# Kernel tuning notes

Measured on AMD Instinct MI355X. Metric: run time of the kernel, lower is better.

The kernel has to match this reference:

```python
import jax, jax.numpy as jnp
import numpy as np

EPS = 1e-6
NUM_HEADS = 12


def ln_cf(x, w, b):
    # channels_first LayerNorm over channel dim (ConvNeXt style)
    u = jnp.mean(x, axis=1, keepdims=True)
    s = jnp.mean((x - u) ** 2, axis=1, keepdims=True)
    xn = (x - u) / jnp.sqrt(s + EPS)
    shp = (1, -1) + (1,) * (x.ndim - 2)
    return xn * w.reshape(shp) + b.reshape(shp)


def conv2s2(x, w):
    # Conv3d kernel=2 stride=2 (no bias): exact non-overlapping patch contraction
    b, c, H, W, D = x.shape
    xp = x.reshape(b, c, H // 2, 2, W // 2, 2, D // 2, 2)
    return jnp.einsum('bchkwpdq,ockpq->bohwd', xp, w)


def convt2s2(x, w):
    # ConvTranspose3d kernel=2 stride=2 (torch weight layout [in, out, 2,2,2])
    b, i, H, W, D = x.shape
    o = w.shape[1]
    y = jnp.einsum('bihwd,iokpq->bohkwpdq', x, w)
    return y.reshape(b, o, 2 * H, 2 * W, 2 * D)


def stem(x, w1, g1, b1, w2, g2, b2):
    h = conv2s2(x, w1)
    h = jax.nn.gelu(ln_cf(h, g1, b1), approximate=False)
    h = conv2s2(h, w2)
    return ln_cf(h, g2, b2)


def debed(x, tw1, g, b, tw2, tb2):
    h = convt2s2(x, tw1)
    h = jax.nn.gelu(ln_cf(h, g, b), approximate=False)
    return convt2s2(h, tw2) + tb2.reshape(1, -1, 1, 1, 1)


def rope(x):
    # rotary embedding over full token dim c (pairs (i, i+c/2)), positions 0..L-1
    b, l, c = x.shape
    inv = 1.0 / (10000.0 ** (jnp.arange(0, c, 2, dtype=jnp.float32) / c))
    t = jnp.arange(l, dtype=jnp.float32)
    f = jnp.outer(t, inv)                      # [l, c/2]
    emb = jnp.concatenate([f, f], axis=-1)     # [l, c]
    cos, sin = jnp.cos(emb)[None], jnp.sin(emb)[None]
    rot = jnp.concatenate([-x[..., c // 2:], x[..., :c // 2]], axis=-1)
    return x * cos + rot * sin


def _forward(x, skip, q_w1, q_g1, q_b1, q_w2, q_g2, q_b2,
             k_w1, k_g1, k_b1, k_w2, k_g2, k_b2,
             v_w1, v_g1, v_b1, v_w2, v_g2, v_b2,
             o_tw1, o_g, o_b, o_tw2, o_tb2,
             ns_w, ns_b, nx_w, nx_b, no_w, no_b):
    res = skip
    skip = ln_cf(skip, ns_w, ns_b)
    x = ln_cf(x, nx_w, nx_b)
    q = stem(skip, q_w1, q_g1, q_b1, q_w2, q_g2, q_b2)
    k = stem(x, k_w1, k_g1, k_b1, k_w2, k_g2, k_b2)
    v = stem(x, v_w1, v_g1, v_b1, v_w2, v_g2, v_b2)
    b, c, Hq, Wq, Dq = q.shape
    _, _, Hk, Wk, Dk = k.shape
    q = q.reshape(b, c, -1).transpose(0, 2, 1)   # [b, Lq, c]
    k = k.reshape(b, c, -1).transpose(0, 2, 1)   # [b, Lk, c]
    v = v.reshape(b, c, -1).transpose(0, 2, 1)
    q = rope(q)
    k = rope(k)
    hd = c // NUM_HEADS
    qh = q.reshape(b, -1, NUM_HEADS, hd).transpose(0, 2, 1, 3)  # [b, nh, Lq, hd]
    kh = k.reshape(b, -1, NUM_HEADS, hd).transpose(0, 2, 1, 3)
    vh = v.reshape(b, -1, NUM_HEADS, hd).transpose(0, 2, 1, 3)
    scale = 1.0 / jnp.sqrt(jnp.float32(hd))
    attn = jax.nn.softmax(jnp.einsum('bhqc,bhkc->bhqk', qh, kh) * scale, axis=-1)
    proj = jnp.einsum('bhqk,bhkc->bhqc', attn, vh)              # [b, nh, Lq, hd]
    # rearrange 'b nh l c -> b (c nh) h w d'
    proj = proj.transpose(0, 3, 1, 2).reshape(b, c, Hq, Wq, Dq)
    proj = ln_cf(proj, no_w, no_b)
    out = debed(proj, o_tw1, o_g, o_b, o_tw2, o_tb2)
    return out + res


def setup_inputs() -> dict:
    key = jax.random.key(0)
    ks = iter(jax.random.split(key, 40))
    def nrm(shape, scale):
        return jax.random.normal(next(ks), shape, jnp.float32) * scale
    E, E4, XF, SF = 768, 192, 6, 6
    inp = {
        'x': nrm((2, XF, 48, 48, 48), 1.0),
        'skip': nrm((2, SF, 48, 48, 48), 1.0),
    }
    for p, ic in [('q', SF), ('k', XF), ('v', XF)]:
        inp[p + '_w1'] = nrm((E4, ic, 2, 2, 2), (ic * 8) ** -0.5)
        inp[p + '_g1'] = jnp.ones(E4, jnp.float32)
        inp[p + '_b1'] = jnp.zeros(E4, jnp.float32)
        inp[p + '_w2'] = nrm((E, E4, 2, 2, 2), (E4 * 8) ** -0.5)
        inp[p + '_g2'] = jnp.ones(E, jnp.float32)
        inp[p + '_b2'] = jnp.zeros(E, jnp.float32)
    inp['o_tw1'] = nrm((E, E4, 2, 2, 2), E ** -0.5)
    inp['o_g'] = jnp.ones(E4, jnp.float32)
    inp['o_b'] = jnp.zeros(E4, jnp.float32)
    inp['o_tw2'] = nrm((E4, SF, 2, 2, 2), E4 ** -0.5)
    inp['o_tb2'] = jnp.zeros(SF, jnp.float32)
    inp['ns_w'] = jnp.ones(SF, jnp.float32)
    inp['ns_b'] = jnp.zeros(SF, jnp.float32)
    inp['nx_w'] = jnp.ones(XF, jnp.float32)
    inp['nx_b'] = jnp.zeros(XF, jnp.float32)
    inp['no_w'] = jnp.ones(E, jnp.float32)
    inp['no_b'] = jnp.zeros(E, jnp.float32)
    return inp


def reference(x, skip, q_w1, q_g1, q_b1, q_w2, q_g2, q_b2,
              k_w1, k_g1, k_b1, k_w2, k_g2, k_b2,
              v_w1, v_g1, v_b1, v_w2, v_g2, v_b2,
              o_tw1, o_g, o_b, o_tw2, o_tb2,
              ns_w, ns_b, nx_w, nx_b, no_w, no_b):
    return _forward(x, skip, q_w1, q_g1, q_b1, q_w2, q_g2, q_b2,
                    k_w1, k_g1, k_b1, k_w2, k_g2, k_b2,
                    v_w1, v_g1, v_b1, v_w2, v_g2, v_b2,
                    o_tw1, o_g, o_b, o_tw2, o_tb2,
                    ns_w, ns_b, nx_w, nx_b, no_w, no_b)
```

## Files before the change

### kernel.cpp

```cpp
#include <hip/hip_runtime.h>
#include <math.h>

#define BB_ 2
#define C0 6
#define S0 48
#define V0 (S0*S0*S0)
#define C1 192
#define S1 24
#define V1 (S1*S1*S1)
#define C2 768
#define S2 12
#define LL (S2*S2*S2)
#define NH 12
#define HD 64
#define KDIM (C1*8)
#define MDIM (BB_*LL)

typedef __attribute__((ext_vector_type(8))) short short8;
typedef __attribute__((ext_vector_type(4))) short short4v;
typedef __attribute__((ext_vector_type(4))) float float4v;

static __device__ __forceinline__ float gelu_exact(float x){
  return 0.5f*x*(1.0f+erff(x*0.70710678118654752440f));
}
static __device__ __forceinline__ unsigned short f2bf(float f){
  unsigned int u = __float_as_uint(f);
  unsigned int r = (u + 0x7fffu + ((u>>16)&1u)) >> 16;
  return (unsigned short)r;
}
static __device__ __forceinline__ unsigned int pk_bf16(float a, float b){
#if __has_builtin(__builtin_amdgcn_cvt_pk_bf16_f32)
  typedef __attribute__((ext_vector_type(2))) __bf16 bf2;
  bf2 r = __builtin_amdgcn_cvt_pk_bf16_f32(a,b);
  union { bf2 v; unsigned int u; } cv; cv.v = r;
  return cv.u;
#else
  return (unsigned int)f2bf(a) | ((unsigned int)f2bf(b)<<16);
#endif
}
static __device__ __forceinline__ float bf2f(unsigned short u){
  return __uint_as_float(((unsigned int)u)<<16);
}
static __device__ __forceinline__ float exp2v(float x){
#if __has_builtin(__builtin_amdgcn_exp2f)
  return __builtin_amdgcn_exp2f(x);
#else
  return exp2f(x);
#endif
}
static __device__ __forceinline__ void load_lds16(const void* g, void* l){
  __builtin_amdgcn_global_load_lds((const __attribute__((address_space(1))) unsigned int*)g,
      (__attribute__((address_space(3))) unsigned int*)l, 16, 0, 0);
}
static __device__ __forceinline__ float4v mfma32(short8 a, short8 b, float4v c){
  return __builtin_amdgcn_mfma_f32_16x16x32_bf16(a,b,c,0,0,0);
}
static __device__ __forceinline__ float4v mfma16(short4v a, short4v b, float4v c){
#if __has_builtin(__builtin_amdgcn_mfma_f32_16x16x16bf16_1k)
  return __builtin_amdgcn_mfma_f32_16x16x16bf16_1k(a,b,c,0,0,0);
#else
  asm volatile("v_mfma_f32_16x16x16_bf16 %0, %1, %2, %0" : "+v"(c) : "v"(a), "v"(b));
  return c;
#endif
}

__global__ __launch_bounds__(256) void prep_kernel(
    const float* __restrict__ skin, const float* __restrict__ xin,
    const float* __restrict__ nsw, const float* __restrict__ nsb,
    const float* __restrict__ nxw, const float* __restrict__ nxb,
    unsigned short* __restrict__ outS, unsigned short* __restrict__ outX,
    const float* __restrict__ qw2, const float* __restrict__ kw2, const float* __restrict__ vw2,
    const float* __restrict__ tw1, const float* __restrict__ tw2,
    const float* __restrict__ qw1, const float* __restrict__ kw1, const float* __restrict__ vw1,
    unsigned short* __restrict__ w2tq, unsigned short* __restrict__ w2tk,
    unsigned short* __restrict__ w2tv, unsigned short* __restrict__ Btd,
    unsigned short* __restrict__ Bt48,
    unsigned short* __restrict__ w1q, unsigned short* __restrict__ w1k,
    unsigned short* __restrict__ w1v){
  int bx = blockIdx.x;
  if (bx < 1728){
    int z = bx >= 864;
    const float* in = z ? xin : skin;
    const float* w  = z ? nxw : nsw;
    const float* bi = z ? nxb : nsb;
    unsigned short* out = z ? outX : outS;
    int idx = (bx - z*864)*256 + threadIdx.x;
    int b = idx / V0, vox = idx - b*V0;
    const float* p = in + (size_t)b*(C0*V0) + vox;
    float v[C0]; float s=0.f;
#pragma unroll
    for (int c=0;c<C0;c++){ v[c]=p[(size_t)c*V0]; s+=v[c]; }
    float u = s*(1.f/C0);
    float ss=0.f;
#pragma unroll
    for (int c=0;c<C0;c++){ float d=v[c]-u; ss+=d*d; }
    float inv = rsqrtf(ss*(1.f/C0)+1e-6f);
    unsigned short* o = out + (size_t)b*(C0*V0) + vox;
#pragma unroll
    for (int c=0;c<C0;c++) o[(size_t)c*V0] = f2bf((v[c]-u)*inv*w[c]+bi[c]);
    return;
  }
  bx -= 1728;
  if (bx < 13824){
    int z = bx/4608;
    int idx = (bx - z*4608)*256 + threadIdx.x;
    const float* w2 = (z==0)?qw2:((z==1)?kw2:vw2);
    unsigned short* o = (z==0)?w2tq:((z==1)?w2tk:w2tv);
    int oc = idx/KDIM; int r = idx-oc*KDIM; int p = r/C1; int ic = r-p*C1;
    o[idx] = f2bf(w2[(size_t)oc*KDIM + ic*8 + p]);
  } else if (bx < 18432){
    int idx = (bx-13824)*256 + threadIdx.x;
    int n = idx/C2; int p = idx-n*C2;
    int i = ((p&63)*NH) + (p>>6);
    int kpq = n/C1, o2 = n-kpq*C1;
    Btd[idx] = f2bf(tw1[(size_t)i*KDIM + o2*8 + kpq]);
  } else if (bx < 18480){
    int idx = (bx-18432)*256 + threadIdx.x;
    int n = idx/C1; int i = idx-n*C1;
    Bt48[idx] = (n<48) ? f2bf(tw2[(size_t)i*48 + n]) : (unsigned short)0;
  } else {
    int idx = (bx-18480)*256 + threadIdx.x;
    int z = idx / 9216; int r = idx - z*9216;
    const float* w1 = (z==0)?qw1:((z==1)?kw1:vw1);
    unsigned short* o = (z==0)?w1q:((z==1)?w1k:w1v);
    o[r] = f2bf(w1[r]);
  }
}

__global__ __launch_bounds__(256) void conv1_kernel(
    const unsigned short* __restrict__ lnSb, const unsigned short* __restrict__ lnXb,
    const unsigned short* __restrict__ w1bq, const unsigned short* __restrict__ w1bk,
    const unsigned short* __restrict__ w1bv,
    const float* __restrict__ qg1, const float* __restrict__ qb1,
    const float* __restrict__ kg1, const float* __restrict__ kb1,
    const float* __restrict__ vg1, const float* __restrict__ vb1,
    unsigned short* __restrict__ h1q, unsigned short* __restrict__ h1k,
    unsigned short* __restrict__ h1v){
  int z = blockIdx.z;
  const unsigned short* in = (z==0)? lnSb : lnXb;
  const unsigned short* Wb = (z==0)?w1bq:((z==1)?w1bk:w1bv);
  const float* g1 = (z==0)?qg1:((z==1)?kg1:vg1);
  const float* b1 = (z==0)?qb1:((z==1)?kb1:vb1);
  unsigned short* h1p = (z==0)?h1q:((z==1)?h1k:h1v);
  int t = threadIdx.x, w = t>>6, lane = t&63;
  int g = lane>>4, l16 = lane&15;
  int j = blockIdx.x*4 + w;
  int bxh = j/18, mt = j - bxh*18;
  int b = bxh/48; int rem = bxh - b*48; int y = rem>>1, xh = rem&1;
  int xo = mt/3, zo = mt - xo*3;
  int xv = xh*12 + xo*2 + (l16>>3);
  int zv = zo*8 + (l16&7);
  int x2 = 2*xv, z2 = 2*zv, y2 = 2*y;
  const unsigned short* base = in + (size_t)b*C0*V0;
  union { short8 v; unsigned int u[4]; } aA;
  {
    size_t rb = (size_t)g*V0;
    aA.u[0] = *(const unsigned int*)&base[rb + (y2+0)*(S0*S0) + (x2+0)*S0 + z2];
    aA.u[1] = *(const unsigned int*)&base[rb + (y2+0)*(S0*S0) + (x2+1)*S0 + z2];
    aA.u[2] = *(const unsigned int*)&base[rb + (y2+1)*(S0*S0) + (x2+0)*S0 + z2];
    aA.u[3] = *(const unsigned int*)&base[rb + (y2+1)*(S0*S0) + (x2+1)*S0 + z2];
  }
  union { short4v v; unsigned int u[2]; } aB;
  {
    size_t rb = (size_t)(4+(g>>1))*V0 + (y2+(g&1))*(S0*S0);
    aB.u[0] = *(const unsigned int*)&base[rb + (x2+0)*S0 + z2];
    aB.u[1] = *(const unsigned int*)&base[rb + (x2+1)*S0 + z2];
  }
  float4v acc[12];
#pragma unroll
  for (int ot=0; ot<12; ot++){
    short8  wA = *(const short8*)&Wb[(ot*16+l16)*48 + g*8];
    short4v wB = *(const short4v*)&Wb[(ot*16+l16)*48 + 32 + g*4];
    float4v a = {};
    a = mfma32(wA, aA.v, a);
    a = mfma16(wB, aB.v, a);
    acc[ot] = a;
  }
  float s1=0.f, s2=0.f;
#pragma unroll
  for (int ot=0;ot<12;ot++)
#pragma unroll
    for (int reg=0;reg<4;reg++){ float v=acc[ot][reg]; s1+=v; s2+=v*v; }
  s1 += __shfl_xor(s1,16); s1 += __shfl_xor(s1,32);
  s2 += __shfl_xor(s2,16); s2 += __shfl_xor(s2,32);
  float u = s1*(1.f/C1);
  float inv = rsqrtf(s2*(1.f/C1)-u*u+1e-6f);
  int tok = (y>>1)*(S2*S2) + (xv>>1)*S2 + (zv>>1);
  int p8 = (y&1)*4 + (xv&1)*2 + (zv&1);
  unsigned short* hb = h1p + (size_t)(b*LL+tok)*KDIM + p8*C1;
#pragma unroll
  for (int ot=0; ot<12; ot++){
    int oc0 = ot*16 + g*4;
    float4 gg = *(const float4*)&g1[oc0];
    float4 bb = *(const float4*)&b1[oc0];
    float x0 = gelu_exact((acc[ot][0]-u)*inv*gg.x+bb.x);
    float x1 = gelu_exact((acc[ot][1]-u)*inv*gg.y+bb.y);
    float x2e= gelu_exact((acc[ot][2]-u)*inv*gg.z+bb.z);
    float x3 = gelu_exact((acc[ot][3]-u)*inv*gg.w+bb.w);
    uint2 pk; pk.x = pk_bf16(x0,x1); pk.y = pk_bf16(x2e,x3);
    *(uint2*)&hb[oc0] = pk;
  }
}

__global__ __launch_bounds__(256) void gemm_stem_kernel(
    const unsigned short* __restrict__ A0, const unsigned short* __restrict__ A1,
    const unsigned short* __restrict__ A2,
    const unsigned short* __restrict__ B0, const unsigned short* __restrict__ B1,
    const unsigned short* __restrict__ B2,
    unsigned short* __restrict__ Cq, unsigned short* __restrict__ Ck,
    unsigned short* __restrict__ Cv){
  int flat = blockIdx.x;
  int xcd = flat & 7, slot = flat >> 3;
  int tile = xcd*61 + slot;
  if (tile >= 486) return;
  int z = tile/162; int rr = tile - z*162;
  int m0 = (rr/6)*128, n0 = (rr - (rr/6)*6)*128;
  const unsigned short* A = (z==0)?A0:((z==1)?A1:A2);
  const unsigned short* Bt = (z==0)?B0:((z==1)?B1:B2);
  unsigned short* Cp = (z==0)?Cq:((z==1)?Ck:Cv);
  __shared__ __align__(16) unsigned short Al[2][128*32];
  __shared__ __align__(16) unsigned short Bl[2][128*32];
  int t=threadIdx.x, w=t>>6, lane=t&63;
  int g=lane>>4, l16=lane&15, r16=lane>>2, c16=lane&3;
  int wm=w>>1, wn=w&1;
  float4v acc[4][4] = {};
#pragma unroll
  for (int cc=0;cc<4;cc++){
    int ch = w*4+cc;
    if (ch<8){
      const unsigned short* gp = A + (size_t)(m0+ch*16+r16)*KDIM + 0 + c16*8;
      load_lds16(gp, &Al[0][ch*512]);
    } else {
      const unsigned short* gp = Bt + (size_t)(n0+(ch-8)*16+r16)*KDIM + 0 + c16*8;
      load_lds16(gp, &Bl[0][(ch-8)*512]);
    }
  }
  __syncthreads();
  int cur = 0;
  for (int kb=0;kb<KDIM;kb+=32){
    if (kb+32 < KDIM){
      int nb = cur^1;
#pragma unroll
      for (int cc=0;cc<4;cc++){
        int ch = w*4+cc;
        if (ch<8){
          const unsigned short* gp = A + (size_t)(m0+ch*16+r16)*KDIM + (kb+32) + c16*8;
          load_lds16(gp, &Al[nb][ch*512]);
        } else {
          const unsigned short* gp = Bt + (size_t)(n0+(ch-8)*16+r16)*KDIM + (kb+32) + c16*8;
          load_lds16(gp, &Bl[nb][(ch-8)*512]);
        }
      }
    }
    short8 af[4], bf[4];
#pragma unroll
    for (int mt=0;mt<4;mt++) af[mt] = *(const short8*)&Al[cur][(wm*64+mt*16+l16)*32 + g*8];
#pragma unroll
    for (int nt=0;nt<4;nt++) bf[nt] = *(const short8*)&Bl[cur][(wn*64+nt*16+l16)*32 + g*8];
#pragma unroll
    for (int mt=0;mt<4;mt++)
#pragma unroll
      for (int nt=0;nt<4;nt++)
        acc[mt][nt] = mfma32(af[mt], bf[nt], acc[mt][nt]);
    __syncthreads();
    cur ^= 1;
  }
#pragma unroll
  for (int mt=0;mt<4;mt++){
    int mb = m0 + wm*64 + mt*16 + g*4;
#pragma unroll
    for (int nt=0;nt<4;nt++){
      int col = n0 + wn*64 + nt*16 + l16;
#pragma unroll
      for (int reg=0;reg<4;reg++)
        Cp[(size_t)(mb+reg)*C2 + col] = f2bf(acc[mt][nt][reg]);
    }
  }
}

__global__ __launch_bounds__(256) void gemm_debed_kernel(const unsigned short* __restrict__ A,
    const unsigned short* __restrict__ Bt, unsigned short* __restrict__ C){
  int flat = blockIdx.x;
  int xcd = flat & 7, slot = flat >> 3;
  int tile = xcd*41 + slot;
  if (tile >= 324) return;
  int m0 = (tile/12)*128, n0 = (tile - (tile/12)*12)*128;
  __shared__ __align__(16) unsigned short Al[2][128*32];
  __shared__ __align__(16) unsigned short Bl[2][128*32];
  int t=threadIdx.x, w=t>>6, lane=t&63;
  int g=lane>>4, l16=lane&15, r16=lane>>2, c16=lane&3;
  int wm=w>>1, wn=w&1;
  float4v acc[4][4] = {};
#pragma unroll
  for (int cc=0;cc<4;cc++){
    int ch = w*4+cc;
    if (ch<8){
      const unsigned short* gp = A + (size_t)(m0+ch*16+r16)*C2 + 0 + c16*8;
      load_lds16(gp, &Al[0][ch*512]);
    } else {
      const unsigned short* gp = Bt + (size_t)(n0+(ch-8)*16+r16)*C2 + 0 + c16*8;
      load_lds16(gp, &Bl[0][(ch-8)*512]);
    }
  }
  __syncthreads();
  int cur = 0;
  for (int kb=0;kb<C2;kb+=32){
    if (kb+32 < C2){
      int nb = cur^1;
#pragma unroll
      for (int cc=0;cc<4;cc++){
        int ch = w*4+cc;
        if (ch<8){
          const unsigned short* gp = A + (size_t)(m0+ch*16+r16)*C2 + (kb+32) + c16*8;
          load_lds16(gp, &Al[nb][ch*512]);
        } else {
          const unsigned short* gp = Bt + (size_t)(n0+(ch-8)*16+r16)*C2 + (kb+32) + c16*8;
          load_lds16(gp, &Bl[nb][(ch-8)*512]);
        }
      }
    }
    short8 af[4], bf[4];
#pragma unroll
    for (int mt=0;mt<4;mt++) af[mt] = *(const short8*)&Al[cur][(wm*64+mt*16+l16)*32 + g*8];
#pragma unroll
    for (int nt=0;nt<4;nt++) bf[nt] = *(const short8*)&Bl[cur][(wn*64+nt*16+l16)*32 + g*8];
#pragma unroll
    for (int mt=0;mt<4;mt++)
#pragma unroll
      for (int nt=0;nt<4;nt++)
        acc[mt][nt] = mfma32(af[mt], bf[nt], acc[mt][nt]);
    __syncthreads();
    cur ^= 1;
  }
#pragma unroll
  for (int nt=0;nt<4;nt++){
    int n = n0 + wn*64 + nt*16 + l16;
    int kpq = n / C1;
    int o = n - kpq*C1;
#pragma unroll
    for (int mt=0;mt<4;mt++){
      int mb = m0 + wm*64 + mt*16 + g*4;
#pragma unroll
      for (int reg=0;reg<4;reg++){
        int m = mb + reg;
        int b = m / LL; int tok = m - b*LL;
        int h = tok/(S2*S2), ww=(tok/S2)%S2, d=tok%S2;
        int v24 = (2*h+((kpq>>2)&1))*(S1*S1) + (2*ww+((kpq>>1)&1))*S1 + (2*d+(kpq&1));
        C[(size_t)(b*V1+v24)*C1 + o] = f2bf(acc[mt][nt][reg]);
      }
    }
  }
}

__global__ __launch_bounds__(256) void final_kernel(const unsigned short* __restrict__ dh,
    const unsigned short* __restrict__ Bt48, const float* __restrict__ og,
    const float* __restrict__ ob, const float* __restrict__ tb2s,
    const float* __restrict__ skipp, float* __restrict__ out){
  __shared__ __align__(16) unsigned short As[64*200];
  __shared__ __align__(16) unsigned short Bs[64*200];
  int t=threadIdx.x, w=t>>6, lane=t&63;
  int g=lane>>4, l16=lane&15;
  int m0 = blockIdx.x*64;
  for (int n8 = t; n8 < 1536; n8 += 256){
    int n64 = n8/24, kk = (n8 - n64*24)*8;
    uint4 d4 = *(const uint4*)&Bt48[n64*192 + kk];
    *(uint4*)&Bs[n64*200 + kk] = d4;
  }
  float g0=og[lane], g1v=og[lane+64], g2v=og[lane+128];
  float b0=ob[lane], b1v=ob[lane+64], b2v=ob[lane+128];
  for (int rr=0; rr<16; rr++){
    int rl = w*16 + rr;
    const unsigned short* row = dh + (size_t)(m0+rl)*C1;
    float v0=bf2f(row[lane]), v1=bf2f(row[lane+64]), v2=bf2f(row[lane+128]);
    float s1=v0+v1+v2, s2=v0*v0+v1*v1+v2*v2;
#pragma unroll
    for (int off=32;off>0;off>>=1){ s1+=__shfl_xor(s1,off); s2+=__shfl_xor(s2,off); }
    float u=s1*(1.f/C1), inv=rsqrtf(s2*(1.f/C1)-u*u+1e-6f);
    As[rl*200+lane]     = f2bf(gelu_exact((v0-u)*inv*g0+b0));
    As[rl*200+lane+64]  = f2bf(gelu_exact((v1-u)*inv*g1v+b1v));
    As[rl*200+lane+128] = f2bf(gelu_exact((v2-u)*inv*g2v+b2v));
  }
  __syncthreads();
  int wm=w>>1, wn=w&1;
  float4v acc[2][2] = {};
#pragma unroll
  for (int kb=0;kb<192;kb+=32){
    short8 af[2], bf[2];
#pragma unroll
    for (int mt=0;mt<2;mt++) af[mt] = *(const short8*)&As[(wm*32+mt*16+l16)*200 + kb + g*8];
#pragma unroll
    for (int nt=0;nt<2;nt++) bf[nt] = *(const short8*)&Bs[(wn*32+nt*16+l16)*200 + kb + g*8];
#pragma unroll
    for (int mt=0;mt<2;mt++)
#pragma unroll
      for (int nt=0;nt<2;nt++)
        acc[mt][nt] = mfma32(af[mt], bf[nt], acc[mt][nt]);
  }
#pragma unroll
  for (int nt=0;nt<2;nt++){
    int n = wn*32 + nt*16 + l16;
    if (n < 48){
      int c = n>>3, kpq = n&7;
      float bias = tb2s[c];
#pragma unroll
      for (int mt=0;mt<2;mt++){
        int mb = m0 + wm*32 + mt*16 + g*4;
#pragma unroll
        for (int reg=0;reg<4;reg++){
          int m = mb + reg;
          int b = m / V1; int v24 = m - b*V1;
          int y24 = v24/(S1*S1), x24=(v24/S1)%S1, z24=v24%S1;
          int vox = (2*y24+((kpq>>2)&1))*(S0*S0) + (2*x24+((kpq>>1)&1))*S0 + 2*z24+(kpq&1);
          size_t oi = (size_t)(b*C0+c)*V0 + vox;
          out[oi] = acc[mt][nt][reg] + bias + skipp[oi];
        }
      }
    }
  }
}

__global__ __launch_bounds__(64) void ln768_stem_kernel(
    unsigned short* __restrict__ qb, unsigned short* __restrict__ kb2,
    unsigned short* __restrict__ vb,
    const float* __restrict__ qg, const float* __restrict__ qbi,
    const float* __restrict__ kg, const float* __restrict__ kbi,
    const float* __restrict__ vg, const float* __restrict__ vbi, float qscale){
  int z = blockIdx.y;
  unsigned short* buf = (z==0)?qb:((z==1)?kb2:vb);
  const float* g  = (z==0)?qg:((z==1)?kg:vg);
  const float* bia= (z==0)?qbi:((z==1)?kbi:vbi);
  float scale = (z==0)? qscale : 1.0f;
  int tok = blockIdx.x, lane = threadIdx.x;
  unsigned short* row = buf + (size_t)tok*C2;
  float v[12]; float s1=0.f,s2=0.f;
#pragma unroll
  for (int i=0;i<12;i++){ float t=bf2f(row[i*64+lane]); v[i]=t; s1+=t; s2+=t*t; }
#pragma unroll
  for (int off=32;off>0;off>>=1){ s1+=__shfl_xor(s1,off); s2+=__shfl_xor(s2,off); }
  float u=s1*(1.f/C2);
  float inv=rsqrtf(s2*(1.f/C2)-u*u+1e-6f);
  if (z==2){
#pragma unroll
    for (int i=0;i<12;i++){ int j=i*64+lane; row[j]=f2bf((v[i]-u)*inv*g[j]+bia[j]); }
  } else {
    int pos = tok % LL;
#pragma unroll
    for (int i=0;i<6;i++){
      int j=i*64+lane;
      float xn1=(v[i]-u)*inv*g[j]+bia[j];
      float xn2=(v[i+6]-u)*inv*g[j+384]+bia[j+384];
      float fr=(float)pos*__expf(-0.02398526139f*(float)j);
      float cs=cosf(fr), sn=sinf(fr);
      row[j]     = f2bf((xn1*cs - xn2*sn)*scale);
      row[j+384] = f2bf((xn2*cs + xn1*sn)*scale);
    }
  }
}

__global__ __launch_bounds__(256) void vtrans_kernel(const unsigned short* __restrict__ vbf,
    unsigned short* __restrict__ vT){
  __shared__ unsigned short T[64*72];
  int tok0 = blockIdx.x*64;
  int h = blockIdx.y, b = blockIdx.z;
  int t = threadIdx.x;
#pragma unroll
  for (int i=0;i<2;i++){
    int idx = t + i*256;
    int token = idx>>3, dc = idx&7;
    uint4 d4 = *(const uint4*)&vbf[(size_t)(b*LL+tok0+token)*C2 + h*64 + dc*8];
    const unsigned short* s = (const unsigned short*)&d4;
#pragma unroll
    for (int j2=0;j2<8;j2++) T[(dc*8+j2)*72 + token] = s[j2];
  }
  __syncthreads();
  int r = t>>2, seg = t&3;
  unsigned short* dst = vT + (size_t)((b*NH+h)*HD + r)*LL + tok0 + seg*16;
  uint4 o[2];
  unsigned short* os = (unsigned short*)o;
#pragma unroll
  for (int j2=0;j2<16;j2++) os[j2] = T[r*72 + seg*16 + j2];
  *(uint4*)dst = o[0];
  *(uint4*)(dst+8) = o[1];
}

__global__ __launch_bounds__(256) void attn_kernel(const unsigned short* __restrict__ q,
    const unsigned short* __restrict__ k, const unsigned short* __restrict__ vt,
    unsigned short* __restrict__ opart, float* __restrict__ lbuf){
  __shared__ __align__(16) unsigned char smem[32768];
  unsigned short* Ks = (unsigned short*)smem;
  unsigned short* Vs = Ks + 4096;
  int flat = blockIdx.x;
  int xcd = flat & 7, slot = flat >> 3;
  int tile = xcd*108 + slot;
  int h = tile / 72; int rem = tile - h*72;
  int zb = rem / 9, qt = rem - zb*9;
  int b = zb >> 2, split = zb & 3;
  int t=threadIdx.x, w=t>>6, lane=t&63;
  int g=lane>>4, l16=lane&15;
  short8 qA[3], qB[3];
#pragma unroll
  for (int j=0;j<3;j++){
    const unsigned short* qrow = q + (size_t)(b*LL + qt*192 + w*48 + j*16 + l16)*C2 + h*64;
    qA[j] = *(const short8*)(qrow + g*8);
    qB[j] = *(const short8*)(qrow + 32 + g*8);
  }
  const unsigned short* kbase = k + (size_t)(b*LL)*C2 + h*64;
  const unsigned short* vbase = vt + (size_t)((b*NH+h)*HD)*LL;
  int sub = lane>>3;
  int chs = (lane&7) ^ sub;
  int ktb = split*7, kte = (split==3)? 27 : (split*7+7);
  const unsigned short* gptr[4];
  unsigned short* ldst[4];
  int gstep[4];
#pragma unroll
  for (int cc=0;cc<4;cc++){
    int ii = w*4+cc;
    if (ii<8){
      int key = ktb*64 + ii*8 + sub;
      gptr[cc] = kbase + (size_t)key*C2 + chs*8;
      gstep[cc] = 64*C2;
      ldst[cc] = &Ks[ii*512];
    } else {
      int d = (ii-8)*8 + sub;
      gptr[cc] = vbase + (size_t)d*LL + ktb*64 + chs*8;
      gstep[cc] = 64;
      ldst[cc] = &Vs[(ii-8)*512];
    }
  }
  int sw = l16 & 7;
  const unsigned short* ksrow = &Ks[l16*64 + (g^sw)*8];
  int c2d = (((4+g)^sw) - (g^sw))*8;
  const unsigned short* vsrow = &Vs[l16*64 + (g&1)*4];
  int xk[4];
#pragma unroll
  for (int kc=0;kc<4;kc++) xk[kc] = (((kc*2 + (g>>1)) ^ sw))*8;
  short4v vones;
  vones[0]=vones[1]=vones[2]=vones[3]=(short)0x3F80;
  float4v O4[3][4] = {};
  float4v Ol[3] = {};
#pragma unroll
  for (int cc=0;cc<4;cc++){
    load_lds16(gptr[cc], ldst[cc]);
    gptr[cc] += gstep[cc];
  }
  __syncthreads();
  int cur = 0;
  for (int kt=ktb; kt<kte; kt++){
    if (kt+1 < kte){
      int so = (cur^1)*8192;
#pragma unroll
      for (int cc=0;cc<4;cc++){
        load_lds16(gptr[cc], ldst[cc]+so);
        gptr[cc] += gstep[cc];
      }
    }
    int co = cur*8192;
    const unsigned short* kr = ksrow + co;
    const unsigned short* vr = vsrow + co;
    float4v sc[3][4];
#pragma unroll
    for (int nt=0;nt<4;nt++){
      short8 k1 = *(const short8*)(kr + nt*1024);
      short8 k2 = *(const short8*)(kr + nt*1024 + c2d);
#pragma unroll
      for (int j=0;j<3;j++){
        float4v zz = {};
        zz = mfma32(k1, qA[j], zz);
        zz = mfma32(k2, qB[j], zz);
        sc[j][nt] = zz;
      }
    }
#pragma unroll
    for (int j=0;j<3;j++)
#pragma unroll
      for (int nt=0;nt<4;nt++)
#pragma unroll
        for (int reg=0;reg<4;reg++)
          sc[j][nt][reg] = exp2v(sc[j][nt][reg]);
    short4v pbs[3][4];
#pragma unroll
    for (int j=0;j<3;j++)
#pragma unroll
      for (int kc=0;kc<4;kc++){
        union { short4v v; unsigned int u[2]; } pb;
        pb.u[0] = pk_bf16(sc[j][kc][0], sc[j][kc][1]);
        pb.u[1] = pk_bf16(sc[j][kc][2], sc[j][kc][3]);
        pbs[j][kc] = pb.v;
      }
#pragma unroll
    for (int kc=0;kc<4;kc++){
      const unsigned short* vp = vr + xk[kc];
      short4v va[4];
#pragma unroll
      for (int dt=0;dt<4;dt++) va[dt] = *(const short4v*)(vp + dt*1024);
#pragma unroll
      for (int j=0;j<3;j++){
        Ol[j] = mfma16(vones, pbs[j][kc], Ol[j]);
#pragma unroll
        for (int dt=0;dt<4;dt++)
          O4[j][dt] = mfma16(va[dt], pbs[j][kc], O4[j][dt]);
      }
    }
    __syncthreads();
    cur ^= 1;
  }
  float* Ot = (float*)smem;
  float* ot = Ot + w*1216;
  int qq = lane>>2, c4 = lane&3;
#pragma unroll
  for (int j=0;j<3;j++){
#pragma unroll
    for (int dt=0;dt<4;dt++)
      *(float4*)&ot[l16*76 + dt*16 + g*4] =
          make_float4(O4[j][dt][0],O4[j][dt][1],O4[j][dt][2],O4[j][dt][3]);
    if (g==0){
      int qi = qt*192 + w*48 + j*16 + l16;
      lbuf[((size_t)(b*4+split)*NH+h)*LL + qi] = Ol[j][0];
    }
    unsigned short* orow = opart + (size_t)split*MDIM*C2
                + (size_t)(b*LL + qt*192 + w*48 + j*16 + qq)*C2 + h*64;
#pragma unroll
    for (int p=0;p<4;p++){
      float4 vv = *(float4*)&ot[qq*76 + p*16 + c4*4];
      uint2 pk; pk.x = pk_bf16(vv.x,vv.y); pk.y = pk_bf16(vv.z,vv.w);
      *(uint2*)&orow[p*16 + c4*4] = pk;
    }
    __syncthreads();
  }
}

__global__ __launch_bounds__(256) void attn_post_kernel(const unsigned short* __restrict__ opart,
    const float* __restrict__ lbuf,
    const float* __restrict__ g, const float* __restrict__ bia,
    unsigned short* __restrict__ aob){
  int t=threadIdx.x, w=t>>6, lane=t&63;
  int m = blockIdx.x*4 + w;
  int b = m / LL, l = m - b*LL;
  const unsigned short* o0 = opart + (size_t)m*C2;
  unsigned short* orow = aob + (size_t)m*C2;
  float vv[12]; float s1=0.f, s2=0.f;
#pragma unroll
  for (int i=0;i<12;i++){
    float ls = 0.f;
#pragma unroll
    for (int s=0;s<4;s++) ls += lbuf[((size_t)(b*4+s)*NH+i)*LL + l];
    float inv = 1.f/ls;
    int j = i*64+lane;
    float val = 0.f;
#pragma unroll
    for (int s=0;s<4;s++) val += bf2f(o0[(size_t)s*MDIM*C2 + j]);
    val *= inv;
    vv[i]=val; s1+=val; s2+=val*val;
  }
#pragma unroll
  for (int off=32;off>0;off>>=1){ s1+=__shfl_xor(s1,off); s2+=__shfl_xor(s2,off); }
  float u=s1*(1.f/C2);
  float invs=rsqrtf(s2*(1.f/C2)-u*u+1e-6f);
#pragma unroll
  for (int i=0;i<12;i++){
    int cj = lane*NH + i;
    orow[i*64+lane] = f2bf((vv[i]-u)*invs*g[cj]+bia[cj]);
  }
}

extern "C" void kernel_launch(void* const* d_in, const int* in_sizes, int n_in,
                              void* d_out, int out_size, void* d_ws, size_t ws_size,
                              hipStream_t stream){
  (void)in_sizes; (void)n_in; (void)out_size; (void)ws_size;
  const float* x    =(const float*)d_in[0];
  const float* skip =(const float*)d_in[1];
  const float* q_w1 =(const float*)d_in[2];
  const float* q_g1 =(const float*)d_in[3];
  const float* q_b1 =(const float*)d_in[4];
  const float* q_w2 =(const float*)d_in[5];
  const float* q_g2 =(const float*)d_in[6];
  const float* q_b2 =(const float*)d_in[7];
  const float* k_w1 =(const float*)d_in[8];
  const float* k_g1 =(const float*)d_in[9];
  const float* k_b1 =(const float*)d_in[10];
  const float* k_w2 =(const float*)d_in[11];
  const float* k_g2 =(const float*)d_in[12];
  const float* k_b2 =(const float*)d_in[13];
  const float* v_w1 =(const float*)d_in[14];
  const float* v_g1 =(const float*)d_in[15];
  const float* v_b1 =(const float*)d_in[16];
  const float* v_w2 =(const float*)d_in[17];
  const float* v_g2 =(const float*)d_in[18];
  const float* v_b2 =(const float*)d_in[19];
  const float* o_tw1=(const float*)d_in[20];
  const float* o_g  =(const float*)d_in[21];
  const float* o_b  =(const float*)d_in[22];
  const float* o_tw2=(const float*)d_in[23];
  const float* o_tb2=(const float*)d_in[24];
  const float* ns_w =(const float*)d_in[25];
  const float* ns_b =(const float*)d_in[26];
  const float* nx_w =(const float*)d_in[27];
  const float* nx_b =(const float*)d_in[28];
  const float* no_w =(const float*)d_in[29];
  const float* no_b =(const float*)d_in[30];
  float* out=(float*)d_out;

  char* W = (char*)d_ws;
  unsigned short* lnSb = (unsigned short*)(W + 0);
  unsigned short* lnXb = (unsigned short*)(W + 2654208);
  unsigned short* h1q  = (unsigned short*)(W + 5308416);
  unsigned short* h1k  = (unsigned short*)(W + 15925248);
  unsigned short* h1v  = (unsigned short*)(W + 26542080);
  unsigned short* w2tq = (unsigned short*)(W + 37158912);
  unsigned short* w2tk = (unsigned short*)(W + 39518208);
  unsigned short* w2tv = (unsigned short*)(W + 41877504);
  unsigned short* qbf  = (unsigned short*)(W + 44236800);
  unsigned short* kbf  = (unsigned short*)(W + 49545216);
  unsigned short* vbf  = (unsigned short*)(W + 54853632);
  unsigned short* vT   = (unsigned short*)(W + 60162048);
  unsigned short* aob  = (unsigned short*)(W + 65470464);
  unsigned short* Btd  = (unsigned short*)(W + 70778880);
  unsigned short* Bt48 = (unsigned short*)(W + 73138176);
  unsigned short* w1q  = (unsigned short*)(W + 73162752);
  unsigned short* w1k  = (unsigned short*)(W + 73181184);
  unsigned short* w1v  = (unsigned short*)(W + 73199616);
  float* lbuf  = (float*)(W + 0);
  unsigned short* opart = (unsigned short*)(W + 5308416);
  unsigned short* dh   = (unsigned short*)(W + 5308416);

  const float QSCALE = 0.125f*1.44269504089f;

  prep_kernel<<<20316,256,0,stream>>>(skip, x, ns_w, ns_b, nx_w, nx_b, lnSb, lnXb,
      q_w2,k_w2,v_w2,o_tw1,o_tw2, q_w1,k_w1,v_w1,
      w2tq,w2tk,w2tv,Btd,Bt48, w1q,w1k,w1v);
  conv1_kernel<<<dim3(432,1,3),256,0,stream>>>(lnSb,lnXb, w1q,w1k,w1v,
      q_g1,q_b1, k_g1,k_b1, v_g1,v_b1, h1q,h1k,h1v);
  gemm_stem_kernel<<<488,256,0,stream>>>(h1q,h1k,h1v,
      w2tq,w2tk,w2tv, qbf,kbf,vbf);
  ln768_stem_kernel<<<dim3(MDIM,3),64,0,stream>>>(qbf,kbf,vbf,
      q_g2,q_b2, k_g2,k_b2, v_g2,v_b2, QSCALE);
  vtrans_kernel<<<dim3(27,12,2),256,0,stream>>>(vbf, vT);
  attn_kernel<<<864,256,0,stream>>>(qbf, kbf, vT, opart, lbuf);
  attn_post_kernel<<<864,256,0,stream>>>(opart, lbuf, no_w, no_b, aob);
  gemm_debed_kernel<<<328,256,0,stream>>>(aob, Btd, dh);
  final_kernel<<<432,256,0,stream>>>(dh, Bt48, o_g, o_b, o_tb2, skip, out);
}
```

Measured before the change: 325.0 us.

## Halve GEMM N-tiles, add XOR-swizzled LDS layout, batch 4 tokens per LN block

Both the stem and debed GEMMs drop from 128x128 to 128x64 tiles, which doubles the grid to fill more CUs. The LDS staging uses an XOR swizzle on the 16-byte column chunk to cut bank conflicts on the short8 fragment reads. The stem LayerNorm kernel now processes 4 tokens per 256-thread block instead of one token per 64-thread block, reducing the block count. Smaller tiles mean less reuse per loaded A tile and more global traffic for A, and the debed kernel drops its tile bounds check because the new grid divides exactly (648 = 8*81).

```diff
diff --git a/kernel.cpp b/kernel.cpp
--- a/kernel.cpp
+++ b/kernel.cpp
@@ -211,29 +211,26 @@
     unsigned short* __restrict__ Cv){
   int flat = blockIdx.x;
   int xcd = flat & 7, slot = flat >> 3;
-  int tile = xcd*61 + slot;
-  if (tile >= 486) return;
-  int z = tile/162; int rr = tile - z*162;
-  int m0 = (rr/6)*128, n0 = (rr - (rr/6)*6)*128;
+  int tile = xcd*122 + slot;
+  if (tile >= 972) return;
+  int z = tile/324; int rr = tile - z*324;
+  int m0 = (rr/12)*128, n0 = (rr - (rr/12)*12)*64;
   const unsigned short* A = (z==0)?A0:((z==1)?A1:A2);
   const unsigned short* Bt = (z==0)?B0:((z==1)?B1:B2);
   unsigned short* Cp = (z==0)?Cq:((z==1)?Ck:Cv);
   __shared__ __align__(16) unsigned short Al[2][128*32];
-  __shared__ __align__(16) unsigned short Bl[2][128*32];
+  __shared__ __align__(16) unsigned short Bl[2][64*32];
   int t=threadIdx.x, w=t>>6, lane=t&63;
   int g=lane>>4, l16=lane&15, r16=lane>>2, c16=lane&3;
   int wm=w>>1, wn=w&1;
-  float4v acc[4][4] = {};
-#pragma unroll
-  for (int cc=0;cc<4;cc++){
-    int ch = w*4+cc;
-    if (ch<8){
-      const unsigned short* gp = A + (size_t)(m0+ch*16+r16)*KDIM + 0 + c16*8;
-      load_lds16(gp, &Al[0][ch*512]);
-    } else {
-      const unsigned short* gp = Bt + (size_t)(n0+(ch-8)*16+r16)*KDIM + 0 + c16*8;
-      load_lds16(gp, &Bl[0][(ch-8)*512]);
-    }
+  int csrc = (c16 ^ ((r16>>1)&3))*8;
+  int crd  = (g   ^ ((l16>>1)&3))*8;
+  float4v acc[4][2] = {};
+#pragma unroll
+  for (int cc=0;cc<3;cc++){
+    int ch = w*3+cc;
+    if (ch<8) load_lds16(A + (size_t)(m0+ch*16+r16)*KDIM + csrc, &Al[0][ch*512]);
+    else      load_lds16(Bt + (size_t)(n0+(ch-8)*16+r16)*KDIM + csrc, &Bl[0][(ch-8)*512]);
   }
   __syncthreads();
   int cur = 0;
@@ -241,26 +238,21 @@
     if (kb+32 < KDIM){
       int nb = cur^1;
 #pragma unroll
-      for (int cc=0;cc<4;cc++){
-        int ch = w*4+cc;
-        if (ch<8){
-          const unsigned short* gp = A + (size_t)(m0+ch*16+r16)*KDIM + (kb+32) + c16*8;
-          load_lds16(gp, &Al[nb][ch*512]);
-        } else {
-          const unsigned short* gp = Bt + (size_t)(n0+(ch-8)*16+r16)*KDIM + (kb+32) + c16*8;
-          load_lds16(gp, &Bl[nb][(ch-8)*512]);
-        }
+      for (int cc=0;cc<3;cc++){
+        int ch = w*3+cc;
+        if (ch<8) load_lds16(A + (size_t)(m0+ch*16+r16)*KDIM + (kb+32) + csrc, &Al[nb][ch*512]);
+        else      load_lds16(Bt + (size_t)(n0+(ch-8)*16+r16)*KDIM + (kb+32) + csrc, &Bl[nb][(ch-8)*512]);
       }
     }
-    short8 af[4], bf[4];
-#pragma unroll
-    for (int mt=0;mt<4;mt++) af[mt] = *(const short8*)&Al[cur][(wm*64+mt*16+l16)*32 + g*8];
-#pragma unroll
-    for (int nt=0;nt<4;nt++) bf[nt] = *(const short8*)&Bl[cur][(wn*64+nt*16+l16)*32 + g*8];
+    short8 af[4], bf[2];
+#pragma unroll
+    for (int mt=0;mt<4;mt++) af[mt] = *(const short8*)&Al[cur][(wm*64+mt*16+l16)*32 + crd];
+#pragma unroll
+    for (int nt=0;nt<2;nt++) bf[nt] = *(const short8*)&Bl[cur][(wn*32+nt*16+l16)*32 + crd];
 #pragma unroll
     for (int mt=0;mt<4;mt++)
 #pragma unroll
-      for (int nt=0;nt<4;nt++)
+      for (int nt=0;nt<2;nt++)
         acc[mt][nt] = mfma32(af[mt], bf[nt], acc[mt][nt]);
     __syncthreads();
     cur ^= 1;
@@ -269,8 +261,8 @@
   for (int mt=0;mt<4;mt++){
     int mb = m0 + wm*64 + mt*16 + g*4;
 #pragma unroll
-    for (int nt=0;nt<4;nt++){
-      int col = n0 + wn*64 + nt*16 + l16;
+    for (int nt=0;nt<2;nt++){
+      int col = n0 + wn*32 + nt*16 + l16;
 #pragma unroll
       for (int reg=0;reg<4;reg++)
         Cp[(size_t)(mb+reg)*C2 + col] = f2bf(acc[mt][nt][reg]);
@@ -282,25 +274,21 @@
     const unsigned short* __restrict__ Bt, unsigned short* __restrict__ C){
   int flat = blockIdx.x;
   int xcd = flat & 7, slot = flat >> 3;
-  int tile = xcd*41 + slot;
-  if (tile >= 324) return;
-  int m0 = (tile/12)*128, n0 = (tile - (tile/12)*12)*128;
+  int tile = xcd*81 + slot;
+  int m0 = (tile/24)*128, n0 = (tile - (tile/24)*24)*64;
   __shared__ __align__(16) unsigned short Al[2][128*32];
-  __shared__ __align__(16) unsigned short Bl[2][128*32];
+  __shared__ __align__(16) unsigned short Bl[2][64*32];
   int t=threadIdx.x, w=t>>6, lane=t&63;
   int g=lane>>4, l16=lane&15, r16=lane>>2, c16=lane&3;
   int wm=w>>1, wn=w&1;
-  float4v acc[4][4] = {};
-#pragma unroll
-  for (int cc=0;cc<4;cc++){
-    int ch = w*4+cc;
-    if (ch<8){
-      const unsigned short* gp = A + (size_t)(m0+ch*16+r16)*C2 + 0 + c16*8;
-      load_lds16(gp, &Al[0][ch*512]);
-    } else {
-      const unsigned short* gp = Bt + (size_t)(n0+(ch-8)*16+r16)*C2 + 0 + c16*8;
-      load_lds16(gp, &Bl[0][(ch-8)*512]);
-    }
+  int csrc = (c16 ^ ((r16>>1)&3))*8;
+  int crd  = (g   ^ ((l16>>1)&3))*8;
+  float4v acc[4][2] = {};
+#pragma unroll
+  for (int cc=0;cc<3;cc++){
+    int ch = w*3+cc;
+    if (ch<8) load_lds16(A + (size_t)(m0+ch*16+r16)*C2 + csrc, &Al[0][ch*512]);
+    else      load_lds16(Bt + (size_t)(n0+(ch-8)*16+r16)*C2 + csrc, &Bl[0][(ch-8)*512]);
   }
   __syncthreads();
   int cur = 0;
@@ -308,33 +296,28 @@
     if (kb+32 < C2){
       int nb = cur^1;
 #pragma unroll
-      for (int cc=0;cc<4;cc++){
-        int ch = w*4+cc;
-        if (ch<8){
-          const unsigned short* gp = A + (size_t)(m0+ch*16+r16)*C2 + (kb+32) + c16*8;
-          load_lds16(gp, &Al[nb][ch*512]);
-        } else {
-          const unsigned short* gp = Bt + (size_t)(n0+(ch-8)*16+r16)*C2 + (kb+32) + c16*8;
-          load_lds16(gp, &Bl[nb][(ch-8)*512]);
-        }
+      for (int cc=0;cc<3;cc++){
+        int ch = w*3+cc;
+        if (ch<8) load_lds16(A + (size_t)(m0+ch*16+r16)*C2 + (kb+32) + csrc, &Al[nb][ch*512]);
+        else      load_lds16(Bt + (size_t)(n0+(ch-8)*16+r16)*C2 + (kb+32) + csrc, &Bl[nb][(ch-8)*512]);
       }
     }
-    short8 af[4], bf[4];
-#pragma unroll
-    for (int mt=0;mt<4;mt++) af[mt] = *(const short8*)&Al[cur][(wm*64+mt*16+l16)*32 + g*8];
-#pragma unroll
-    for (int nt=0;nt<4;nt++) bf[nt] = *(const short8*)&Bl[cur][(wn*64+nt*16+l16)*32 + g*8];
+    short8 af[4], bf[2];
+#pragma unroll
+    for (int mt=0;mt<4;mt++) af[mt] = *(const short8*)&Al[cur][(wm*64+mt*16+l16)*32 + crd];
+#pragma unroll
+    for (int nt=0;nt<2;nt++) bf[nt] = *(const short8*)&Bl[cur][(wn*32+nt*16+l16)*32 + crd];
 #pragma unroll
     for (int mt=0;mt<4;mt++)
 #pragma unroll
-      for (int nt=0;nt<4;nt++)
+      for (int nt=0;nt<2;nt++)
         acc[mt][nt] = mfma32(af[mt], bf[nt], acc[mt][nt]);
     __syncthreads();
     cur ^= 1;
   }
 #pragma unroll
-  for (int nt=0;nt<4;nt++){
-    int n = n0 + wn*64 + nt*16 + l16;
+  for (int nt=0;nt<2;nt++){
+    int n = n0 + wn*32 + nt*16 + l16;
     int kpq = n / C1;
     int o = n - kpq*C1;
 #pragma unroll
@@ -419,7 +402,7 @@
   }
 }
 
-__global__ __launch_bounds__(64) void ln768_stem_kernel(
+__global__ __launch_bounds__(256) void ln768_stem_kernel(
     unsigned short* __restrict__ qb, unsigned short* __restrict__ kb2,
     unsigned short* __restrict__ vb,
     const float* __restrict__ qg, const float* __restrict__ qbi,
@@ -430,7 +413,7 @@
   const float* g  = (z==0)?qg:((z==1)?kg:vg);
   const float* bia= (z==0)?qbi:((z==1)?kbi:vbi);
   float scale = (z==0)? qscale : 1.0f;
-  int tok = blockIdx.x, lane = threadIdx.x;
+  int tok = blockIdx.x*4 + (threadIdx.x>>6), lane = threadIdx.x&63;
   unsigned short* row = buf + (size_t)tok*C2;
   float v[12]; float s1=0.f,s2=0.f;
 #pragma unroll
@@ -730,13 +713,13 @@
       w2tq,w2tk,w2tv,Btd,Bt48, w1q,w1k,w1v);
   conv1_kernel<<<dim3(432,1,3),256,0,stream>>>(lnSb,lnXb, w1q,w1k,w1v,
       q_g1,q_b1, k_g1,k_b1, v_g1,v_b1, h1q,h1k,h1v);
-  gemm_stem_kernel<<<488,256,0,stream>>>(h1q,h1k,h1v,
+  gemm_stem_kernel<<<976,256,0,stream>>>(h1q,h1k,h1v,
       w2tq,w2tk,w2tv, qbf,kbf,vbf);
-  ln768_stem_kernel<<<dim3(MDIM,3),64,0,stream>>>(qbf,kbf,vbf,
+  ln768_stem_kernel<<<dim3(864,3),256,0,stream>>>(qbf,kbf,vbf,
       q_g2,q_b2, k_g2,k_b2, v_g2,v_b2, QSCALE);
   vtrans_kernel<<<dim3(27,12,2),256,0,stream>>>(vbf, vT);
   attn_kernel<<<864,256,0,stream>>>(qbf, kbf, vT, opart, lbuf);
   attn_post_kernel<<<864,256,0,stream>>>(opart, lbuf, no_w, no_b, aob);
-  gemm_debed_kernel<<<328,256,0,stream>>>(aob, Btd, dh);
+  gemm_debed_kernel<<<648,256,0,stream>>>(aob, Btd, dh);
   final_kernel<<<432,256,0,stream>>>(dh, Bt48, o_g, o_b, o_tb2, skip, out);
 }
```

After: 326.3 us. No clear change (+0.4%).
